# Kernel optimization log

Hardware: AMD Instinct MI355X
Metric: run time of the kernel (lower is better)

Reference implementation:

```python
import jax, jax.numpy as jnp
import numpy as np

B, C, F, K = 16, 1000, 256, 10
IPM_ITERS = 20   # fixed-iteration primal-dual interior point (qpth eps=0.01 analogue)
SIGMA = 0.1      # centering parameter
MARGIN = 0.05


def setup_inputs() -> dict:
    key = jax.random.key(0)
    ks = jax.random.split(key, 6)
    logits_pred = jax.random.normal(ks[0], (B, C), jnp.float32)
    feats_pred = jax.random.normal(ks[1], (B, F), jnp.float32)
    feats_pred_0 = jax.random.normal(ks[2], (B, F), jnp.float32)
    head_W = jax.random.normal(ks[3], (C, F), jnp.float32) * 0.05
    head_bias = jax.random.normal(ks[4], (C,), jnp.float32) * 0.05
    # K distinct attack-target classes per sample (order defines the desired ranking)
    perm = jax.vmap(lambda k: jax.random.permutation(k, C))(jax.random.split(ks[5], B))
    attack_targets = perm[:, :K].astype(jnp.int32)
    margin = jnp.full((1,), MARGIN, jnp.float32)
    return {"logits_pred": logits_pred, "feats_pred": feats_pred,
            "feats_pred_0": feats_pred_0, "attack_targets": attack_targets,
            "head_W": head_W, "head_bias": head_bias, "margin": margin}


def build_D(attack_targets):
    # replicates the torch scatter/index_put sequence, in the same overwrite order
    col = jnp.arange(C)
    t_last = attack_targets[:, -1]
    base = -jnp.eye(C, dtype=jnp.float32)[None]                       # (B,C,C) via broadcast
    D = jnp.where(col[None, None, :] == t_last[:, None, None], 1.0, base)
    row_mask = (jnp.arange(C)[None, :, None] == attack_targets[:, None, :]).any(-1)  # (B,C)
    D = jnp.where(row_mask[:, :, None], 0.0, D)
    bi = jnp.broadcast_to(jnp.arange(B)[:, None], (B, K - 1))
    t_pos = attack_targets[:, :-1]
    t_neg = attack_targets[:, 1:]
    D = D.at[bi, t_neg, t_neg].set(-1.0)
    D = D.at[bi, t_neg, t_pos].set(1.0)
    return D


def solve_qp_ipm(p, G, h):
    # min_z z'z + p'z  s.t. G z <= h   (Q = 2*I), infeasible-start primal-dual IPM
    Bn, m, n = G.shape
    z = -0.5 * p                       # unconstrained minimizer (anchor feats)
    s = jnp.ones((Bn, m), p.dtype)
    lam = jnp.ones((Bn, m), p.dtype)
    eye_n = jnp.eye(n, dtype=p.dtype)
    big = jnp.asarray(1e10, p.dtype)

    def step(carry, _):
        z, lam, s = carry
        mu = (lam * s).mean(-1, keepdims=True)
        rd = 2.0 * z + p + jnp.einsum('bm,bmn->bn', lam, G)
        rp = jnp.einsum('bmn,bn->bm', G, z) + s - h
        rc = lam * s - SIGMA * mu
        w = lam / s
        M = 2.0 * eye_n + jnp.einsum('bmi,bm,bmj->bij', G, w, G)   # (B,n,n) KKT Schur
        rhs = -(rd + jnp.einsum('bmi,bm->bi', G, (lam * rp - rc) / s))
        dz = jnp.linalg.solve(M, rhs[..., None])[..., 0]
        ds = -rp - jnp.einsum('bmn,bn->bm', G, dz)
        dlam = -(rc + lam * ds) / s
        a1 = jnp.where(ds < 0, -s / ds, big).min(-1)
        a2 = jnp.where(dlam < 0, -lam / dlam, big).min(-1)
        alpha = jnp.minimum(1.0, 0.99 * jnp.minimum(a1, a2))[:, None]
        return (z + alpha * dz, lam + alpha * dlam, s + alpha * ds), None

    (z, lam, s), _ = jax.lax.scan(step, (z, lam, s), None, length=IPM_ITERS)
    return z


def reference(logits_pred, feats_pred, feats_pred_0, attack_targets, head_W, head_bias, margin):
    D = build_D(attack_targets)                                   # (B,C,C)
    G = -jnp.einsum('bck,kf->bcf', D, head_W)                     # (B,C,F)
    Hc = jnp.einsum('bck,k->bc', D, head_bias) - margin[0]        # = -(margin - D@b)
    Hc = Hc.at[jnp.arange(B), attack_targets[:, 0]].set(0.0)
    P = -2.0 * feats_pred
    z_sol = solve_qp_ipm(P, G, Hc)
    loss = ((feats_pred - z_sol) ** 2).sum(-1)                    # (B,)
    return loss
```

## Files before the change

### kernel.cpp

```cpp
#include <hip/hip_runtime.h>


#define B_N 16
#define C_N 1000
#define F_N 256
#define ITERS_N 20
#define SIGMA_C 0.1f
#define BIGV 1e10f

static const size_t OFF_WT  = 0;
static const size_t OFF_X   = 256000;
static const size_t OFF_M64 = 4352000;
static const size_t OFF_H   = 6449152;
static const size_t OFF_LAM = OFF_H   + 16000;
static const size_t OFF_S   = OFF_LAM + 16000;
static const size_t OFF_RP  = OFF_S   + 16000;
static const size_t OFF_RC  = OFF_RP  + 16000;
static const size_t OFF_WV  = OFF_RC  + 16000;
static const size_t OFF_Z   = OFF_WV  + 16000;
static const size_t OFF_DZ  = OFF_Z   + 4096;
static const size_t OFF_RHS = OFF_DZ  + 4096;
static const size_t OFF_AI  = OFF_RHS + 4096;
static const size_t OFF_BI  = OFF_AI  + 16000;

__device__ __forceinline__ float bsum256(float v, float* red) {
#pragma unroll
  for (int o = 32; o > 0; o >>= 1) v += __shfl_down(v, o);
  __syncthreads();
  if ((threadIdx.x & 63) == 0) red[threadIdx.x >> 6] = v;
  __syncthreads();
  return red[0] + red[1] + red[2] + red[3];
}
__device__ __forceinline__ float bmin256(float v, float* red) {
#pragma unroll
  for (int o = 32; o > 0; o >>= 1) v = fminf(v, __shfl_down(v, o));
  __syncthreads();
  if ((threadIdx.x & 63) == 0) red[threadIdx.x >> 6] = v;
  __syncthreads();
  return fminf(fminf(red[0], red[1]), fminf(red[2], red[3]));
}

__global__ __launch_bounds__(256) void k_transpose(const float* __restrict__ W,
                                                   float* __restrict__ WT) {
  __shared__ float tile[64][65];
  int tc = blockIdx.x & 15, tk = blockIdx.x >> 4;
  int c0 = tc * 64, k0 = tk * 64;
  int t = threadIdx.x;
  int jj = t & 63, r4 = t >> 6;
#pragma unroll
  for (int i = 0; i < 16; ++i) {
    int r = r4 + i * 4;
    int c = c0 + r;
    tile[r][jj] = (c < C_N) ? W[c * F_N + k0 + jj] : 0.f;
  }
  __syncthreads();
#pragma unroll
  for (int i = 0; i < 16; ++i) {
    int kr = r4 + i * 4;
    int cc = c0 + jj;
    if (cc < C_N) WT[(k0 + kr) * C_N + cc] = tile[jj][kr];
  }
}

__global__ __launch_bounds__(256) void k_setup(const int* __restrict__ tg,
                                               const float* __restrict__ bias,
                                               const float* __restrict__ feats,
                                               const float* __restrict__ marg,
                                               float* wsf) {
  int b = blockIdx.x, t = threadIdx.x;
  __shared__ int tsh[10];
  if (t < 10) tsh[t] = tg[b * 10 + t];
  __syncthreads();
  float m = marg[0];
  int t9 = tsh[9];
  float bias_t9 = bias[t9];
  int*   ai  = (int*)(wsf + OFF_AI) + b * C_N;
  int*   bi  = (int*)(wsf + OFF_BI) + b * C_N;
  float* h   = wsf + OFF_H   + b * C_N;
  float* lam = wsf + OFF_LAM + b * C_N;
  float* s   = wsf + OFF_S   + b * C_N;
#pragma unroll
  for (int r = 0; r < 4; ++r) {
    int c = t + 256 * r;
    if (c < C_N) {
      int rk = -1;
#pragma unroll
      for (int i = 0; i < 10; ++i) if (c == tsh[i]) rk = i;
      int av, bv; float hv;
      if (rk < 0)       { av = c;        bv = t9;         hv = bias_t9 - bias[c] - m; }
      else if (rk == 0) { av = 0;        bv = 0;          hv = 0.f; }
      else              { av = tsh[rk];  bv = tsh[rk-1];  hv = bias[tsh[rk-1]] - bias[tsh[rk]] - m; }
      ai[c] = av; bi[c] = bv; h[c] = hv; lam[c] = 1.f; s[c] = 1.f;
    }
  }
  (wsf + OFF_Z)[b * F_N + t] = feats[b * F_N + t];
}

__global__ __launch_bounds__(256) void k_buildX(const float* __restrict__ W,
                                                float* wsf) {
  int bb = blockIdx.x >> 3, part = blockIdx.x & 7;
  int t = threadIdx.x;
  __shared__ int aL[125], bL[125];
  int c0 = part * 125;
  const int* ai = (const int*)(wsf + OFF_AI) + bb * C_N;
  const int* bi = (const int*)(wsf + OFF_BI) + bb * C_N;
  if (t < 125) { aL[t] = ai[c0 + t]; bL[t] = bi[c0 + t]; }
  __syncthreads();
  float* X = wsf + OFF_X + (size_t)bb * 256000 + (size_t)c0 * F_N;
  for (int i = 0; i < 125; ++i) {
    float wa = W[aL[i] * F_N + t];
    float wb = W[bL[i] * F_N + t];
    X[i * F_N + t] = wa - wb;
  }
}

__global__ __launch_bounds__(256) void k_iter_pre(const float* __restrict__ W,
                                                  const float* __restrict__ feats,
                                                  const int* __restrict__ tg,
                                                  float* wsf, int do_update) {
  int b = blockIdx.x, t = threadIdx.x;
  __shared__ float zs[256], dzs[256];
  __shared__ __align__(16) float ys[1000];
  __shared__ float vs[1000];
  __shared__ float red[4];
  __shared__ int tsh[10];

  const float* WT = wsf + OFF_WT;
  const int* ai  = (const int*)(wsf + OFF_AI) + b * C_N;
  const int* bi  = (const int*)(wsf + OFF_BI) + b * C_N;
  float* h    = wsf + OFF_H   + b * C_N;
  float* lam  = wsf + OFF_LAM + b * C_N;
  float* s    = wsf + OFF_S   + b * C_N;
  float* rp   = wsf + OFF_RP  + b * C_N;
  float* rc   = wsf + OFF_RC  + b * C_N;
  float* wbuf = wsf + OFF_WV  + b * C_N;
  float* z    = wsf + OFF_Z   + b * F_N;
  float* dz   = wsf + OFF_DZ  + b * F_N;
  float* rhs  = wsf + OFF_RHS + b * F_N;

  if (t < 10) tsh[t] = tg[b * 10 + t];
  zs[t] = z[t];
  if (do_update) dzs[t] = dz[t];
  __syncthreads();

  float lamr[4], sr[4], rpr[4];
  if (do_update) {
    if (t < 250) {
      float4 acc = make_float4(0.f, 0.f, 0.f, 0.f);
      const float4* WT4 = (const float4*)WT;
#pragma unroll 4
      for (int k = 0; k < 256; ++k) {
        float zk = dzs[k];
        float4 w4 = WT4[k * 250 + t];
        acc.x += zk * w4.x; acc.y += zk * w4.y; acc.z += zk * w4.z; acc.w += zk * w4.w;
      }
      *(float4*)&ys[4 * t] = acc;
    }
    __syncthreads();
    float amin = BIGV;
    float dsr[4], dlr[4];
#pragma unroll
    for (int r = 0; r < 4; ++r) {
      int c = t + 256 * r;
      if (c < C_N) {
        float lv = lam[c], sv = s[c], rpv = rp[c], rcv = rc[c];
        float g = ys[ai[c]] - ys[bi[c]];
        float dsv = -rpv - g;
        float dlv = -(rcv + lv * dsv) / sv;
        if (dsv < 0.f) amin = fminf(amin, -sv / dsv);
        if (dlv < 0.f) amin = fminf(amin, -lv / dlv);
        lamr[r] = lv; sr[r] = sv; dsr[r] = dsv; dlr[r] = dlv;
      }
    }
    float am = bmin256(amin, red);
    float alpha = fminf(1.f, 0.99f * am);
#pragma unroll
    for (int r = 0; r < 4; ++r) {
      int c = t + 256 * r;
      if (c < C_N) {
        lamr[r] += alpha * dlr[r];
        sr[r]   += alpha * dsr[r];
        lam[c] = lamr[r]; s[c] = sr[r];
      }
    }
    zs[t] += alpha * dzs[t];
    z[t] = zs[t];
    __syncthreads();
  } else {
#pragma unroll
    for (int r = 0; r < 4; ++r) {
      int c = t + 256 * r;
      if (c < C_N) { lamr[r] = lam[c]; sr[r] = s[c]; }
    }
  }

  if (t < 250) {
    float4 acc = make_float4(0.f, 0.f, 0.f, 0.f);
    const float4* WT4 = (const float4*)WT;
#pragma unroll 4
    for (int k = 0; k < 256; ++k) {
      float zk = zs[k];
      float4 w4 = WT4[k * 250 + t];
      acc.x += zk * w4.x; acc.y += zk * w4.y; acc.z += zk * w4.z; acc.w += zk * w4.w;
    }
    *(float4*)&ys[4 * t] = acc;
  }
  __syncthreads();

  float musum = 0.f;
#pragma unroll
  for (int r = 0; r < 4; ++r) {
    int c = t + 256 * r;
    if (c < C_N) {
      float g = ys[ai[c]] - ys[bi[c]];
      rpr[r] = g + sr[r] - h[c];
      musum += lamr[r] * sr[r];
    }
  }
  float mu = bsum256(musum, red) * (1.f / 1000.f);

  float vsum = 0.f;
#pragma unroll
  for (int r = 0; r < 4; ++r) {
    int c = t + 256 * r;
    if (c < C_N) {
      float prod = lamr[r] * sr[r];
      float rcv = prod - SIGMA_C * mu;
      rc[c] = rcv; rp[c] = rpr[r];
      wbuf[c] = lamr[r] / sr[r];
      float vv = lamr[r] + (lamr[r] * rpr[r] - rcv) / sr[r];
      vs[c] = vv; vsum += vv;
    }
  }
  float S_all = bsum256(vsum, red);

  float vt[10];
#pragma unroll
  for (int i = 0; i < 10; ++i) vt[i] = vs[tsh[i]];
  float S_tgt = 0.f;
#pragma unroll
  for (int i = 0; i < 10; ++i) S_tgt += vt[i];
  float S_gen = S_all - S_tgt;
  __syncthreads();

#pragma unroll
  for (int r = 0; r < 4; ++r) {
    int c = t + 256 * r;
    if (c < C_N) {
      int rk = -1;
#pragma unroll
      for (int i = 0; i < 10; ++i) if (c == tsh[i]) rk = i;
      float vc = vs[c];
      float u;
      if (rk < 0)        u = vc;
      else if (rk == 0)  u = -vt[1];
      else if (rk < 9)   u = vc - vt[rk + 1];
      else               u = vc - S_gen;
      vs[c] = u;
    }
  }
  __syncthreads();

  {
    float acc = 0.f;
#pragma unroll 4
    for (int c = 0; c < C_N; ++c) acc += vs[c] * W[c * F_N + t];
    rhs[t] = -(2.f * zs[t] - 2.f * feats[b * F_N + t] + acc);
  }
}

__global__ __launch_bounds__(256) void k_syrk(float* wsf) {
  int blk = blockIdx.x;
  int b = blk / 10, tile = blk % 10;
  const int TI[10] = {0,1,1,2,2,2,3,3,3,3};
  const int TJ[10] = {0,0,1,0,1,2,0,1,2,3};
  int ti = TI[tile], tj = TJ[tile];
  int t = threadIdx.x;
  int tx = t & 15, ty = t >> 4;
  __shared__ __align__(16) float As[64][64];
  __shared__ __align__(16) float Bs[64][64];
  const float* X  = wsf + OFF_X  + (size_t)b * 256000;
  const float* wv = wsf + OFF_WV + b * C_N;
  float acc[4][4] = {{0.f}};
  int f4 = t & 15, jr0 = t >> 4;
  for (int cc = 0; cc < C_N; cc += 64) {
    __syncthreads();
#pragma unroll
    for (int rep = 0; rep < 4; ++rep) {
      int j = jr0 + rep * 16;
      int c = cc + j;
      float wj = (c < C_N) ? wv[c] : 0.f;
      float4 v = (c < C_N) ? *(const float4*)&X[(size_t)c * F_N + ti * 64 + f4 * 4]
                           : make_float4(0.f, 0.f, 0.f, 0.f);
      float4 u;
      if (tj == ti) u = v;
      else u = (c < C_N) ? *(const float4*)&X[(size_t)c * F_N + tj * 64 + f4 * 4]
                         : make_float4(0.f, 0.f, 0.f, 0.f);
      float4 vw = make_float4(wj * v.x, wj * v.y, wj * v.z, wj * v.w);
      *(float4*)&As[j][f4 * 4] = vw;
      *(float4*)&Bs[j][f4 * 4] = u;
    }
    __syncthreads();
#pragma unroll 4
    for (int j = 0; j < 64; ++j) {
      float4 a4 = *(const float4*)&As[j][tx * 4];
      float4 b4 = *(const float4*)&Bs[j][ty * 4];
      acc[0][0] += a4.x * b4.x; acc[0][1] += a4.x * b4.y; acc[0][2] += a4.x * b4.z; acc[0][3] += a4.x * b4.w;
      acc[1][0] += a4.y * b4.x; acc[1][1] += a4.y * b4.y; acc[1][2] += a4.y * b4.z; acc[1][3] += a4.y * b4.w;
      acc[2][0] += a4.z * b4.x; acc[2][1] += a4.z * b4.y; acc[2][2] += a4.z * b4.z; acc[2][3] += a4.z * b4.w;
      acc[3][0] += a4.w * b4.x; acc[3][1] += a4.w * b4.y; acc[3][2] += a4.w * b4.z; acc[3][3] += a4.w * b4.w;
    }
  }
  double* M64 = (double*)(wsf + OFF_M64) + (size_t)b * 65536;
#pragma unroll
  for (int e = 0; e < 4; ++e) {
    int i = ti * 64 + tx * 4 + e;
    int k0 = tj * 64 + ty * 4;
#pragma unroll
    for (int q = 0; q < 4; ++q) {
      float v = acc[e][q] + ((i == k0 + q) ? 2.f : 0.f);
      M64[(size_t)i * F_N + k0 + q] = (double)v;
    }
  }
}

__global__ __launch_bounds__(512) void k_chol(float* wsf) {
  int b = blockIdx.x, t = threadIdx.x;
  double* M = (double*)(wsf + OFF_M64) + (size_t)b * 65536;
  __shared__ double Sm[8464];
  double* Db   = Sm;
  double* invd = Sm + 272;
  double* Pb   = Sm + 304;
  double* Pu   = Sm + 4384;
  __shared__ double yv[256];
  __shared__ double red2[8][65];

  for (int p = 0; p < 16; ++p) {
    int p0 = p * 16, p1 = p0 + 16, nb = 256 - p1;

    if (t < 16) {
      int l = t;
      double a[16];
#pragma unroll
      for (int q = 0; q < 16; ++q) a[q] = M[(size_t)(p0 + l) * F_N + p0 + q];
#pragma unroll
      for (int j = 0; j < 16; ++j) {
        double d = __shfl(a[j], j);
        double dc = (fabs(d) < 1e-30) ? (d < 0.0 ? -1e-30 : 1e-30) : d;
        double inv = 1.0 / dc;
        if (l == j) a[j] = dc;
        else if (l > j) a[j] *= inv;
#pragma unroll
        for (int k = j + 1; k < 16; ++k) {
          double lkj = __shfl(a[j], k);
          if (l >= k) a[k] -= a[j] * (lkj * dc);
        }
      }
#pragma unroll
      for (int q = 0; q < 16; ++q) {
        M[(size_t)(p0 + l) * F_N + p0 + q] = a[q];
        Db[l * 17 + q] = a[q];
      }
      invd[l] = 1.0 / a[l];
    }
    __syncthreads();

    if (t < nb) {
      int r = p1 + t;
      double x[16];
#pragma unroll
      for (int q = 0; q < 16; ++q) x[q] = M[(size_t)r * F_N + p0 + q];
#pragma unroll
      for (int k = 0; k < 16; ++k) {
        double uk = x[k];
#pragma unroll
        for (int j = k + 1; j < 16; ++j) x[j] -= uk * Db[j * 17 + k];
        x[k] = uk * invd[k];
        Pu[t * 17 + k] = uk;
        Pb[t * 17 + k] = x[k];
      }
#pragma unroll
      for (int q = 0; q < 16; ++q) M[(size_t)r * F_N + p0 + q] = x[q];
    }
    __syncthreads();

    int nt4 = nb >> 2;
    int Ntile = nt4 * (nt4 + 1) / 2;
    for (int tt = t; tt < Ntile; tt += 512) {
      float fsq = sqrtf((float)(8 * tt + 1));
      int ti = (int)((fsq - 1.f) * 0.5f);
      while ((ti + 1) * (ti + 2) / 2 <= tt) ++ti;
      while (ti * (ti + 1) / 2 > tt) --ti;
      int tk = tt - ti * (ti + 1) / 2;
      int ib = ti * 4, kb = tk * 4;
      double* m0 = M + (size_t)(p1 + ib) * F_N + p1 + kb;
      double a00 = m0[0],       a01 = m0[1],       a02 = m0[2],       a03 = m0[3];
      double a10 = m0[256],     a11 = m0[257],     a12 = m0[258],     a13 = m0[259];
      double a20 = m0[512],     a21 = m0[513],     a22 = m0[514],     a23 = m0[515];
      double a30 = m0[768],     a31 = m0[769],     a32 = m0[770],     a33 = m0[771];
#pragma unroll
      for (int j = 0; j < 16; ++j) {
        double A0 = Pb[(ib + 0) * 17 + j], A1 = Pb[(ib + 1) * 17 + j];
        double A2 = Pb[(ib + 2) * 17 + j], A3 = Pb[(ib + 3) * 17 + j];
        double B0 = Pu[(kb + 0) * 17 + j], B1 = Pu[(kb + 1) * 17 + j];
        double B2 = Pu[(kb + 2) * 17 + j], B3 = Pu[(kb + 3) * 17 + j];
        a00 -= A0 * B0; a01 -= A0 * B1; a02 -= A0 * B2; a03 -= A0 * B3;
        a10 -= A1 * B0; a11 -= A1 * B1; a12 -= A1 * B2; a13 -= A1 * B3;
        a20 -= A2 * B0; a21 -= A2 * B1; a22 -= A2 * B2; a23 -= A2 * B3;
        a30 -= A3 * B0; a31 -= A3 * B1; a32 -= A3 * B2; a33 -= A3 * B3;
      }
      m0[0]   = a00; m0[1]   = a01; m0[2]   = a02; m0[3]   = a03;
      m0[256] = a10; m0[257] = a11; m0[258] = a12; m0[259] = a13;
      m0[512] = a20; m0[513] = a21; m0[514] = a22; m0[515] = a23;
      m0[768] = a30; m0[769] = a31; m0[770] = a32; m0[771] = a33;
    }
    __syncthreads();
  }

  {
    const float* rhs = wsf + OFF_RHS + (size_t)b * F_N;
    if (t < 256) yv[t] = (double)rhs[t];
  }
  __syncthreads();
  double (*Ls)[66] = (double(*)[66])Sm;

  for (int blk = 0; blk < 4; ++blk) {
    int r0 = blk * 64;
    {
      int row = t >> 3, c8 = (t & 7) * 8;
#pragma unroll
      for (int q = 0; q < 8; ++q)
        Ls[row][c8 + q] = M[(size_t)(r0 + row) * F_N + r0 + c8 + q];
    }
    __syncthreads();
    if (t < 64) {
      int l = t;
      double acc = yv[r0 + l];
#pragma unroll
      for (int j = 0; j < 64; ++j) {
        double xj = __shfl(acc, j);
        if (l > j) acc -= Ls[l][j] * xj;
      }
      yv[r0 + l] = acc;
    }
    __syncthreads();
    int nrem = 192 - blk * 64;
    if (t < nrem) {
      int r = r0 + 64 + t;
      double a2 = 0.0;
#pragma unroll 4
      for (int j = 0; j < 64; ++j) a2 += M[(size_t)r * F_N + r0 + j] * yv[r0 + j];
      yv[r] -= a2;
    }
    __syncthreads();
  }

  if (t < 256) yv[t] = yv[t] / M[(size_t)t * F_N + t];
  __syncthreads();

  for (int blk = 3; blk >= 0; --blk) {
    int r0 = blk * 64, r1 = r0 + 64;
    if (blk < 3) {
      int i = r0 + (t & 63), g = t >> 6;
      double part = 0.0;
      for (int j = r1 + g; j < 256; j += 8) part += M[(size_t)j * F_N + i] * yv[j];
      red2[g][t & 63] = part;
      __syncthreads();
      if (t < 64) {
        double tot = 0.0;
#pragma unroll
        for (int g2 = 0; g2 < 8; ++g2) tot += red2[g2][t];
        yv[r0 + t] -= tot;
      }
      __syncthreads();
    }
    {
      int row = t >> 3, c8 = (t & 7) * 8;
#pragma unroll
      for (int q = 0; q < 8; ++q)
        Ls[row][c8 + q] = M[(size_t)(r0 + row) * F_N + r0 + c8 + q];
    }
    __syncthreads();
    if (t < 64) {
      int l = t;
      double acc = yv[r0 + l];
#pragma unroll
      for (int j = 63; j >= 0; --j) {
        double xj = __shfl(acc, j);
        if (l < j) acc -= Ls[j][l] * xj;
      }
      yv[r0 + l] = acc;
    }
    __syncthreads();
  }

  if (t < 256) (wsf + OFF_DZ)[(size_t)b * F_N + t] = (float)yv[t];
}

__global__ __launch_bounds__(256) void k_final(const float* __restrict__ feats,
                                               float* wsf, float* __restrict__ out) {
  int b = blockIdx.x, t = threadIdx.x;
  __shared__ float zs[256], dzs[256];
  __shared__ __align__(16) float ys[1000];
  __shared__ float red[4];
  const float* WT = wsf + OFF_WT;
  const int* ai  = (const int*)(wsf + OFF_AI) + b * C_N;
  const int* bi  = (const int*)(wsf + OFF_BI) + b * C_N;
  const float* lam = wsf + OFF_LAM + b * C_N;
  const float* s   = wsf + OFF_S   + b * C_N;
  const float* rp  = wsf + OFF_RP  + b * C_N;
  const float* rc  = wsf + OFF_RC  + b * C_N;
  const float* z   = wsf + OFF_Z   + b * F_N;
  const float* dz  = wsf + OFF_DZ  + b * F_N;

  zs[t] = z[t];
  dzs[t] = dz[t];
  __syncthreads();
  if (t < 250) {
    float4 acc = make_float4(0.f, 0.f, 0.f, 0.f);
    const float4* WT4 = (const float4*)WT;
#pragma unroll 4
    for (int k = 0; k < 256; ++k) {
      float zk = dzs[k];
      float4 w4 = WT4[k * 250 + t];
      acc.x += zk * w4.x; acc.y += zk * w4.y; acc.z += zk * w4.z; acc.w += zk * w4.w;
    }
    *(float4*)&ys[4 * t] = acc;
  }
  __syncthreads();
  float amin = BIGV;
#pragma unroll
  for (int r = 0; r < 4; ++r) {
    int c = t + 256 * r;
    if (c < C_N) {
      float lv = lam[c], sv = s[c], rpv = rp[c], rcv = rc[c];
      float g = ys[ai[c]] - ys[bi[c]];
      float dsv = -rpv - g;
      float dlv = -(rcv + lv * dsv) / sv;
      if (dsv < 0.f) amin = fminf(amin, -sv / dsv);
      if (dlv < 0.f) amin = fminf(amin, -lv / dlv);
    }
  }
  float am = bmin256(amin, red);
  float alpha = fminf(1.f, 0.99f * am);
  float zf = zs[t] + alpha * dzs[t];
  float d = feats[b * F_N + t] - zf;
  float loss = bsum256(d * d, red);
  if (t == 0) out[b] = loss;
}

extern "C" void kernel_launch(void* const* d_in, const int* in_sizes, int n_in,
                              void* d_out, int out_size, void* d_ws, size_t ws_size,
                              hipStream_t stream) {
  (void)in_sizes; (void)n_in; (void)out_size; (void)ws_size;
  const float* feats = (const float*)d_in[1];
  const int*   tg    = (const int*)d_in[3];
  const float* W     = (const float*)d_in[4];
  const float* bias  = (const float*)d_in[5];
  const float* marg  = (const float*)d_in[6];
  float* wsf = (float*)d_ws;
  float* out = (float*)d_out;

  k_transpose<<<64, 256, 0, stream>>>(W, wsf + OFF_WT);
  k_setup<<<B_N, 256, 0, stream>>>(tg, bias, feats, marg, wsf);
  k_buildX<<<B_N * 8, 256, 0, stream>>>(W, wsf);
  for (int it = 0; it < ITERS_N; ++it) {
    k_iter_pre<<<B_N, 256, 0, stream>>>(W, feats, tg, wsf, it > 0 ? 1 : 0);
    k_syrk<<<B_N * 10, 256, 0, stream>>>(wsf);
    k_chol<<<B_N, 512, 0, stream>>>(wsf);
  }
  k_final<<<B_N, 256, 0, stream>>>(feats, wsf, out);
}
```

Before: 8.556 ms.

## Widen Cholesky panel to 32 columns with 1024 threads and swizzled shared panel

The blocked Cholesky now uses 32-wide panels (8 panel steps instead of 16) and launches 1024 threads per block. It keeps only the unscaled panel in shared memory with an XOR swizzle and applies the inverse diagonal inside the trailing update, which removes the second scaled copy. This halves the number of barrier-separated panel phases and gives more threads to the trailing update. In exchange the serial 32x32 diagonal factorization on a single wavefront grows, and the per-thread 32-element register arrays raise register pressure.

After: 19.75 ms. 2.31x slower.

```diff
diff --git a/kernel.cpp b/kernel.cpp
--- a/kernel.cpp
+++ b/kernel.cpp
@@ -324,42 +324,43 @@
   }
 }
 
-__global__ __launch_bounds__(512) void k_chol(float* wsf) {
+#define PUX(r, j) Pu[(r) * 33 + ((j) ^ (((r) >> 2) & 7))]
+
+__global__ __launch_bounds__(1024) void k_chol(float* wsf) {
   int b = blockIdx.x, t = threadIdx.x;
   double* M = (double*)(wsf + OFF_M64) + (size_t)b * 65536;
-  __shared__ double Sm[8464];
+  __shared__ double Sm[8480];
+  __shared__ double yv[256];
+  __shared__ double red2[16 * 65];
   double* Db   = Sm;
-  double* invd = Sm + 272;
-  double* Pb   = Sm + 304;
-  double* Pu   = Sm + 4384;
-  __shared__ double yv[256];
-  __shared__ double red2[8][65];
-
-  for (int p = 0; p < 16; ++p) {
-    int p0 = p * 16, p1 = p0 + 16, nb = 256 - p1;
-
-    if (t < 16) {
+  double* invd = Sm + 1056;
+  double* Pu   = Sm + 1088;
+
+  for (int p = 0; p < 8; ++p) {
+    int p0 = p * 32, p1 = p0 + 32, nb = 256 - p1;
+
+    if (t < 32) {
       int l = t;
-      double a[16];
-#pragma unroll
-      for (int q = 0; q < 16; ++q) a[q] = M[(size_t)(p0 + l) * F_N + p0 + q];
-#pragma unroll
-      for (int j = 0; j < 16; ++j) {
+      double a[32];
+#pragma unroll
+      for (int q = 0; q < 32; ++q) a[q] = M[(size_t)(p0 + l) * F_N + p0 + q];
+#pragma unroll
+      for (int j = 0; j < 32; ++j) {
         double d = __shfl(a[j], j);
         double dc = (fabs(d) < 1e-30) ? (d < 0.0 ? -1e-30 : 1e-30) : d;
         double inv = 1.0 / dc;
         if (l == j) a[j] = dc;
         else if (l > j) a[j] *= inv;
 #pragma unroll
-        for (int k = j + 1; k < 16; ++k) {
+        for (int k = j + 1; k < 32; ++k) {
           double lkj = __shfl(a[j], k);
           if (l >= k) a[k] -= a[j] * (lkj * dc);
         }
       }
 #pragma unroll
-      for (int q = 0; q < 16; ++q) {
+      for (int q = 0; q < 32; ++q) {
         M[(size_t)(p0 + l) * F_N + p0 + q] = a[q];
-        Db[l * 17 + q] = a[q];
+        Db[l * 33 + q] = a[q];
       }
       invd[l] = 1.0 / a[l];
     }
@@ -367,26 +368,25 @@
 
     if (t < nb) {
       int r = p1 + t;
-      double x[16];
-#pragma unroll
-      for (int q = 0; q < 16; ++q) x[q] = M[(size_t)r * F_N + p0 + q];
-#pragma unroll
-      for (int k = 0; k < 16; ++k) {
+      double x[32];
+#pragma unroll
+      for (int q = 0; q < 32; ++q) x[q] = M[(size_t)r * F_N + p0 + q];
+#pragma unroll
+      for (int k = 0; k < 32; ++k) {
         double uk = x[k];
 #pragma unroll
-        for (int j = k + 1; j < 16; ++j) x[j] -= uk * Db[j * 17 + k];
+        for (int j = k + 1; j < 32; ++j) x[j] -= uk * Db[j * 33 + k];
         x[k] = uk * invd[k];
-        Pu[t * 17 + k] = uk;
-        Pb[t * 17 + k] = x[k];
-      }
-#pragma unroll
-      for (int q = 0; q < 16; ++q) M[(size_t)r * F_N + p0 + q] = x[q];
+        PUX(t, k) = uk;
+      }
+#pragma unroll
+      for (int q = 0; q < 32; ++q) M[(size_t)r * F_N + p0 + q] = x[q];
     }
     __syncthreads();
 
     int nt4 = nb >> 2;
     int Ntile = nt4 * (nt4 + 1) / 2;
-    for (int tt = t; tt < Ntile; tt += 512) {
+    for (int tt = t; tt < Ntile; tt += 1024) {
       float fsq = sqrtf((float)(8 * tt + 1));
       int ti = (int)((fsq - 1.f) * 0.5f);
       while ((ti + 1) * (ti + 2) / 2 <= tt) ++ti;
@@ -394,16 +394,17 @@
       int tk = tt - ti * (ti + 1) / 2;
       int ib = ti * 4, kb = tk * 4;
       double* m0 = M + (size_t)(p1 + ib) * F_N + p1 + kb;
-      double a00 = m0[0],       a01 = m0[1],       a02 = m0[2],       a03 = m0[3];
-      double a10 = m0[256],     a11 = m0[257],     a12 = m0[258],     a13 = m0[259];
-      double a20 = m0[512],     a21 = m0[513],     a22 = m0[514],     a23 = m0[515];
-      double a30 = m0[768],     a31 = m0[769],     a32 = m0[770],     a33 = m0[771];
-#pragma unroll
-      for (int j = 0; j < 16; ++j) {
-        double A0 = Pb[(ib + 0) * 17 + j], A1 = Pb[(ib + 1) * 17 + j];
-        double A2 = Pb[(ib + 2) * 17 + j], A3 = Pb[(ib + 3) * 17 + j];
-        double B0 = Pu[(kb + 0) * 17 + j], B1 = Pu[(kb + 1) * 17 + j];
-        double B2 = Pu[(kb + 2) * 17 + j], B3 = Pu[(kb + 3) * 17 + j];
+      double a00 = m0[0],   a01 = m0[1],   a02 = m0[2],   a03 = m0[3];
+      double a10 = m0[256], a11 = m0[257], a12 = m0[258], a13 = m0[259];
+      double a20 = m0[512], a21 = m0[513], a22 = m0[514], a23 = m0[515];
+      double a30 = m0[768], a31 = m0[769], a32 = m0[770], a33 = m0[771];
+#pragma unroll
+      for (int j = 0; j < 32; ++j) {
+        double dj = invd[j];
+        double A0 = PUX(ib + 0, j), A1 = PUX(ib + 1, j);
+        double A2 = PUX(ib + 2, j), A3 = PUX(ib + 3, j);
+        double B0 = PUX(kb + 0, j) * dj, B1 = PUX(kb + 1, j) * dj;
+        double B2 = PUX(kb + 2, j) * dj, B3 = PUX(kb + 3, j) * dj;
         a00 -= A0 * B0; a01 -= A0 * B1; a02 -= A0 * B2; a03 -= A0 * B3;
         a10 -= A1 * B0; a11 -= A1 * B1; a12 -= A1 * B2; a13 -= A1 * B3;
         a20 -= A2 * B0; a21 -= A2 * B1; a22 -= A2 * B2; a23 -= A2 * B3;
@@ -422,15 +423,15 @@
     if (t < 256) yv[t] = (double)rhs[t];
   }
   __syncthreads();
-  double (*Ls)[66] = (double(*)[66])Sm;
+  double* Ls = Sm;
 
   for (int blk = 0; blk < 4; ++blk) {
     int r0 = blk * 64;
     {
-      int row = t >> 3, c8 = (t & 7) * 8;
-#pragma unroll
-      for (int q = 0; q < 8; ++q)
-        Ls[row][c8 + q] = M[(size_t)(r0 + row) * F_N + r0 + c8 + q];
+      int row = t >> 4, c4 = (t & 15) * 4;
+#pragma unroll
+      for (int q = 0; q < 4; ++q)
+        Ls[row * 66 + c4 + q] = M[(size_t)(r0 + row) * F_N + r0 + c4 + q];
     }
     __syncthreads();
     if (t < 64) {
@@ -439,7 +440,7 @@
 #pragma unroll
       for (int j = 0; j < 64; ++j) {
         double xj = __shfl(acc, j);
-        if (l > j) acc -= Ls[l][j] * xj;
+        if (l > j) acc -= Ls[l * 66 + j] * xj;
       }
       yv[r0 + l] = acc;
     }
@@ -463,22 +464,22 @@
     if (blk < 3) {
       int i = r0 + (t & 63), g = t >> 6;
       double part = 0.0;
-      for (int j = r1 + g; j < 256; j += 8) part += M[(size_t)j * F_N + i] * yv[j];
-      red2[g][t & 63] = part;
+      for (int j = r1 + g; j < 256; j += 16) part += M[(size_t)j * F_N + i] * yv[j];
+      red2[g * 65 + (t & 63)] = part;
       __syncthreads();
       if (t < 64) {
         double tot = 0.0;
 #pragma unroll
-        for (int g2 = 0; g2 < 8; ++g2) tot += red2[g2][t];
+        for (int g2 = 0; g2 < 16; ++g2) tot += red2[g2 * 65 + t];
         yv[r0 + t] -= tot;
       }
       __syncthreads();
     }
     {
-      int row = t >> 3, c8 = (t & 7) * 8;
-#pragma unroll
-      for (int q = 0; q < 8; ++q)
-        Ls[row][c8 + q] = M[(size_t)(r0 + row) * F_N + r0 + c8 + q];
+      int row = t >> 4, c4 = (t & 15) * 4;
+#pragma unroll
+      for (int q = 0; q < 4; ++q)
+        Ls[row * 66 + c4 + q] = M[(size_t)(r0 + row) * F_N + r0 + c4 + q];
     }
     __syncthreads();
     if (t < 64) {
@@ -487,7 +488,7 @@
 #pragma unroll
       for (int j = 63; j >= 0; --j) {
         double xj = __shfl(acc, j);
-        if (l < j) acc -= Ls[j][l] * xj;
+        if (l < j) acc -= Ls[j * 66 + l] * xj;
       }
       yv[r0 + l] = acc;
     }
@@ -567,7 +568,7 @@
   for (int it = 0; it < ITERS_N; ++it) {
     k_iter_pre<<<B_N, 256, 0, stream>>>(W, feats, tg, wsf, it > 0 ? 1 : 0);
     k_syrk<<<B_N * 10, 256, 0, stream>>>(wsf);
-    k_chol<<<B_N, 512, 0, stream>>>(wsf);
+    k_chol<<<B_N, 1024, 0, stream>>>(wsf);
   }
   k_final<<<B_N, 256, 0, stream>>>(feats, wsf, out);
 }
```
